# Kernel tuning notes

Hardware: AMD Instinct MI355X
Metric: run time of the kernel (lower is better)

Reference implementation:

```python
import jax, jax.numpy as jnp
import numpy as np

H = 2048      # hidden size
E = 16        # num experts
F = 1408      # per-expert ffn
FS = 4096     # shared expert ffn
B, S = 2, 1024


def setup_inputs() -> dict:
    key = jax.random.key(0)
    ks = jax.random.split(key, 9)
    s = 0.02
    x = jax.random.normal(ks[0], (B, S, H), dtype=jnp.float32)
    w_router = jax.random.normal(ks[1], (E, H), dtype=jnp.float32) * s
    Wg = jax.random.normal(ks[2], (E, H, F), dtype=jnp.float32) * s
    Wu = jax.random.normal(ks[3], (E, H, F), dtype=jnp.float32) * s
    Wd = jax.random.normal(ks[4], (E, F, H), dtype=jnp.float32) * s
    Wg_s = jax.random.normal(ks[5], (H, FS), dtype=jnp.float32) * s
    Wu_s = jax.random.normal(ks[6], (H, FS), dtype=jnp.float32) * s
    Wd_s = jax.random.normal(ks[7], (FS, H), dtype=jnp.float32) * s
    return {"x": x, "w_router": w_router, "Wg": Wg, "Wu": Wu, "Wd": Wd,
            "Wg_s": Wg_s, "Wu_s": Wu_s, "Wd_s": Wd_s, "top_k": 4}


def reference(x, w_router, Wg, Wu, Wd, Wg_s, Wu_s, Wd_s, top_k):
    # router: softmax in fp32, top-k, renormalize
    logits = jnp.einsum('bsh,eh->bse', x, w_router)
    probs = jax.nn.softmax(logits.astype(jnp.float32), axis=-1)
    w, idx = jax.lax.top_k(probs, top_k)            # [B,S,K]
    w = w / jnp.sum(w, axis=-1, keepdims=True)
    # per-token weight per expert; top-k experts are distinct, so the
    # per-slot masked loop in torch collapses to a single mask [B,S,E]
    mask = jnp.sum(jax.nn.one_hot(idx, E, dtype=w.dtype) * w[..., None], axis=-2)
    out = jnp.zeros_like(x)
    for e in range(E):
        m = mask[..., e:e + 1]                      # [B,S,1]
        xi = x * m                                  # input scaled by routing weight (matches torch)
        h = jax.nn.silu(jnp.einsum('bsh,hf->bsf', xi, Wg[e])) \
            * jnp.einsum('bsh,hf->bsf', xi, Wu[e])
        out = out + jnp.einsum('bsf,fh->bsh', h, Wd[e]) * m
    # shared expert (always active, unscaled)
    hs = jax.nn.silu(jnp.einsum('bsh,hf->bsf', x, Wg_s)) \
         * jnp.einsum('bsh,hf->bsf', x, Wu_s)
    out = out + jnp.einsum('bsf,fh->bsh', hs, Wd_s)
    return out
```

## Files before the change

kernel.cpp:

```cpp
#include <hip/hip_runtime.h>

#define H 2048
#define E 16
#define F 1408
#define FS 4096
#define T 2048
#define TOPK 4
#define CAP 2048
#define LDA 40
#define NPADROWS (T * TOPK + E * 128)

typedef __bf16 bf16;
typedef bf16 bf16x4 __attribute__((ext_vector_type(4)));
typedef bf16 bf16x8 __attribute__((ext_vector_type(8)));
typedef float floatx4 __attribute__((ext_vector_type(4)));

static __device__ __forceinline__ floatx4 mfma16(bf16x8 a, bf16x8 b, floatx4 c) {
    return __builtin_amdgcn_mfma_f32_16x16x32_bf16(a, b, c, 0, 0, 0);
}

static __device__ __forceinline__ void gload16(const bf16* g, bf16* l) {
    __builtin_amdgcn_global_load_lds(
        (const __attribute__((address_space(1))) void*)g,
        (__attribute__((address_space(3))) void*)l, 16, 0, 0);
}

__global__ __launch_bounds__(256) void router_kernel(
    const float* __restrict__ x, const float* __restrict__ wr,
    int* __restrict__ cnt, int* __restrict__ tokid, float* __restrict__ tokw) {
    const int wave = threadIdx.x >> 6;
    const int lane = threadIdx.x & 63;
    const int t = blockIdx.x * 4 + wave;
    if (t >= T) return;
    const float* xrow = x + (size_t)t * H;
    float xr[H / 64];
#pragma unroll
    for (int i = 0; i < H / 64; i++) xr[i] = xrow[lane + i * 64];
    float logits[E];
    for (int e = 0; e < E; e++) {
        const float* wrow = wr + (size_t)e * H;
        float p = 0.f;
#pragma unroll
        for (int i = 0; i < H / 64; i++) p += xr[i] * wrow[lane + i * 64];
        for (int off = 32; off; off >>= 1) p += __shfl_xor(p, off, 64);
        logits[e] = p;
    }
    float mx = logits[0];
    for (int e = 1; e < E; e++) mx = fmaxf(mx, logits[e]);
    float pr[E];
    float sum = 0.f;
    for (int e = 0; e < E; e++) { pr[e] = __expf(logits[e] - mx); sum += pr[e]; }
    float inv = 1.f / sum;
    for (int e = 0; e < E; e++) pr[e] *= inv;
    int sel[TOPK]; float sw[TOPK]; float wsum = 0.f;
    for (int k = 0; k < TOPK; k++) {
        float best = -1.f; int bi = 0;
        for (int e = 0; e < E; e++) if (pr[e] > best) { best = pr[e]; bi = e; }
        sel[k] = bi; sw[k] = best; wsum += best; pr[bi] = -2.f;
    }
    if (lane == 0) {
        float invw = 1.f / wsum;
        for (int k = 0; k < TOPK; k++) {
            int e = sel[k];
            int pos = atomicAdd(&cnt[e], 1);
            tokid[e * CAP + pos] = t;
            tokw[e * CAP + pos] = sw[k] * invw;
        }
    }
}

__global__ void prefix_kernel(const int* __restrict__ cnt, int* __restrict__ prefix, int pad) {
    if (threadIdx.x == 0) {
        int s = 0;
        for (int e = 0; e < E; e++) {
            prefix[e] = s;
            int c = cnt[e];
            s += pad ? ((c + 127) & ~127) : c;
        }
        prefix[E] = s;
    }
}

__global__ __launch_bounds__(256) void convert_x(const float* __restrict__ x,
                                                 bf16* __restrict__ Xb) {
    const int t = threadIdx.x;
    const int row = blockIdx.x * 8 + (t >> 5);
    const int l32 = t & 31;
    const float* src = x + (size_t)row * H;
    bf16* dst = Xb + (size_t)row * H;
    const int xk = (row & 3) << 3;
#pragma unroll
    for (int i = 0; i < 8; i++) {
        int kb = l32 * 8 + i * 256;
        float4 a = *(const float4*)(src + kb);
        float4 b = *(const float4*)(src + kb + 4);
        bf16x8 v;
        v[0] = (bf16)a.x; v[1] = (bf16)a.y; v[2] = (bf16)a.z; v[3] = (bf16)a.w;
        v[4] = (bf16)b.x; v[5] = (bf16)b.y; v[6] = (bf16)b.z; v[7] = (bf16)b.w;
        *(bf16x8*)(dst + (kb ^ xk)) = v;
    }
}

__global__ __launch_bounds__(256) void gather_x(
    const float* __restrict__ x, const int* __restrict__ cnt,
    const int* __restrict__ prefixPad, const int* __restrict__ tokid,
    const float* __restrict__ tokw, bf16* __restrict__ Xg) {
    const int e = blockIdx.y;
    const int s0 = blockIdx.x * 8;
    const int n = cnt[e];
    if (s0 >= n) return;
    const int t = threadIdx.x;
    const int sl = s0 + (t >> 5);
    const int l32 = t & 31;
    if (sl >= n) return;
    const int tok = tokid[e * CAP + sl];
    const float w = tokw[e * CAP + sl];
    const int row = prefixPad[e] + sl;
    const float* src = x + (size_t)tok * H;
    bf16* dst = Xg + (size_t)row * H;
    const int xk = (row & 3) << 3;
#pragma unroll
    for (int i = 0; i < 8; i++) {
        int kb = l32 * 8 + i * 256;
        float4 a = *(const float4*)(src + kb);
        float4 b = *(const float4*)(src + kb + 4);
        bf16x8 v;
        v[0] = (bf16)(a.x * w); v[1] = (bf16)(a.y * w);
        v[2] = (bf16)(a.z * w); v[3] = (bf16)(a.w * w);
        v[4] = (bf16)(b.x * w); v[5] = (bf16)(b.y * w);
        v[6] = (bf16)(b.z * w); v[7] = (bf16)(b.w * w);
        *(bf16x8*)(dst + (kb ^ xk)) = v;
    }
}

__global__ __launch_bounds__(256) void transpose_cvt(
    const float* __restrict__ src, bf16* __restrict__ dst, int R, int C) {
    __shared__ bf16 tile[32][36];
    const int t = threadIdx.x;
    const size_t zb = (size_t)blockIdx.z * R * C;
    const int r0 = blockIdx.y * 32, c0 = blockIdx.x * 32;
    {
        const int rl = t >> 3, c4 = (t & 7) * 4;
        float4 v = *(const float4*)(src + zb + (size_t)(r0 + rl) * C + c0 + c4);
        tile[rl][c4 + 0] = (bf16)v.x;
        tile[rl][c4 + 1] = (bf16)v.y;
        tile[rl][c4 + 2] = (bf16)v.z;
        tile[rl][c4 + 3] = (bf16)v.w;
    }
    __syncthreads();
    {
        const int cl = t >> 3, r4 = (t & 7) * 4;
        bf16x4 o;
        o[0] = tile[r4 + 0][cl];
        o[1] = tile[r4 + 1][cl];
        o[2] = tile[r4 + 2][cl];
        o[3] = tile[r4 + 3][cl];
        const int cg = c0 + cl;
        *(bf16x4*)(dst + zb + (size_t)cg * R + ((r0 + r4) ^ ((cg & 3) << 3))) = o;
    }
}

template <bool EXPERT>
__global__ __launch_bounds__(256, 2) void s1_gemm(
    const bf16* __restrict__ Abuf, const bf16* __restrict__ BgT,
    const bf16* __restrict__ BuT, bf16* __restrict__ hout,
    const int* __restrict__ cnt, const int* __restrict__ prefixPad, int nF) {
    __shared__ __align__(16) bf16 As[128 * 32];
    __shared__ __align__(16) bf16 Bgs[128 * 32];
    __shared__ __align__(16) bf16 Bus[128 * 32];
    const int tid = threadIdx.x;
    const int n0 = blockIdx.x * 128;
    const int m0 = blockIdx.y * 128;
    int ne = T;
    const bf16* A = Abuf;
    const bf16* bg = BgT;
    const bf16* bu = BuT;
    bf16* hb = hout;
    if (EXPERT) {
        const int e = blockIdx.z;
        ne = cnt[e];
        if (m0 >= ne) return;
        const int pp = prefixPad[e];
        A = Abuf + (size_t)pp * H;
        bg = BgT + (size_t)e * F * H;
        bu = BuT + (size_t)e * F * H;
        hb = hout + (size_t)pp * F;
    }
    const int lane = tid & 63;
    const int wave = tid >> 6;
    const int sr = wave * 32 + (lane >> 2);
    const int sc = (lane & 3) * 8;
    const int lo = wave * 1024;
    const bf16* aSrc = A + (size_t)(m0 + sr) * H + sc;
    const bf16* gSrc = bg + (size_t)(n0 + sr) * H + sc;
    const bf16* uSrc = bu + (size_t)(n0 + sr) * H + sc;

    const int m_ = lane & 15;
    const int quad = lane >> 4;
    const int wm = (wave & 1) * 64;
    const int wn = (wave >> 1) * 64;
    const int xq = (quad ^ (m_ & 3)) << 3;

    floatx4 accg[4][4], accu[4][4];
#pragma unroll
    for (int i = 0; i < 4; i++)
#pragma unroll
        for (int j = 0; j < 4; j++) {
            accg[i][j] = (floatx4){0.f, 0.f, 0.f, 0.f};
            accu[i][j] = (floatx4){0.f, 0.f, 0.f, 0.f};
        }

    for (int k0 = 0; k0 < H; k0 += 32) {
        gload16(aSrc + k0, &As[lo]);
        gload16(aSrc + k0 + (size_t)16 * H, &As[lo + 512]);
        gload16(gSrc + k0, &Bgs[lo]);
        gload16(gSrc + k0 + (size_t)16 * H, &Bgs[lo + 512]);
        gload16(uSrc + k0, &Bus[lo]);
        gload16(uSrc + k0 + (size_t)16 * H, &Bus[lo + 512]);
        __syncthreads();
        bf16x8 af[4], bgf[4], buf_[4];
#pragma unroll
        for (int mi = 0; mi < 4; mi++)
            af[mi] = *(const bf16x8*)&As[(wm + mi * 16 + m_) * 32 + xq];
#pragma unroll
        for (int ni = 0; ni < 4; ni++) {
            bgf[ni] = *(const bf16x8*)&Bgs[(wn + ni * 16 + m_) * 32 + xq];
            buf_[ni] = *(const bf16x8*)&Bus[(wn + ni * 16 + m_) * 32 + xq];
        }
#pragma unroll
        for (int mi = 0; mi < 4; mi++)
#pragma unroll
            for (int ni = 0; ni < 4; ni++) {
                accg[mi][ni] = mfma16(af[mi], bgf[ni], accg[mi][ni]);
                accu[mi][ni] = mfma16(af[mi], buf_[ni], accu[mi][ni]);
            }
        __syncthreads();
    }

#pragma unroll
    for (int mi = 0; mi < 4; mi++)
#pragma unroll
        for (int ni = 0; ni < 4; ni++)
#pragma unroll
            for (int r = 0; r < 4; r++) {
                int row = m0 + wm + mi * 16 + quad * 4 + r;
                int col = n0 + wn + ni * 16 + m_;
                if (!EXPERT || row < ne) {
                    float g = accg[mi][ni][r];
                    float u = accu[mi][ni][r];
                    float hv = g / (1.f + __expf(-g)) * u;
                    hb[(size_t)row * nF + (col ^ ((row & 3) << 3))] = (bf16)hv;
                }
            }
}

template <bool EXPERT>
__global__ __launch_bounds__(256, 3) void s2_gemm(
    const bf16* __restrict__ hin, const bf16* __restrict__ BdT,
    float* __restrict__ out, const int* __restrict__ cnt,
    const int* __restrict__ prefixPad, const int* __restrict__ tokid,
    const float* __restrict__ tokw, int nK) {
    __shared__ __align__(16) bf16 As[128 * 32];
    __shared__ __align__(16) bf16 Bs[128 * 32];
    const int tid = threadIdx.x;
    const int n0 = blockIdx.x * 128;
    const int m0 = blockIdx.y * 128;
    int ne = T;
    const bf16* hb = hin;
    const bf16* bd = BdT;
    int e = 0;
    if (EXPERT) {
        e = blockIdx.z;
        ne = cnt[e];
        if (m0 >= ne) return;
        hb = hin + (size_t)prefixPad[e] * F;
        bd = BdT + (size_t)e * F * H;
    }
    const int lane = tid & 63;
    const int wave = tid >> 6;
    const int sr = wave * 32 + (lane >> 2);
    const int sc = (lane & 3) * 8;
    const int lo = wave * 1024;
    const bf16* aSrc = hb + (size_t)(m0 + sr) * nK + sc;
    const bf16* bSrc = bd + (size_t)(n0 + sr) * nK + sc;

    const int m_ = lane & 15;
    const int quad = lane >> 4;
    const int wm = (wave & 1) * 64;
    const int wn = (wave >> 1) * 64;
    const int xq = (quad ^ (m_ & 3)) << 3;

    floatx4 acc[4][4];
#pragma unroll
    for (int i = 0; i < 4; i++)
#pragma unroll
        for (int j = 0; j < 4; j++) acc[i][j] = (floatx4){0.f, 0.f, 0.f, 0.f};

    for (int k0 = 0; k0 < nK; k0 += 32) {
        gload16(aSrc + k0, &As[lo]);
        gload16(aSrc + k0 + (size_t)16 * nK, &As[lo + 512]);
        gload16(bSrc + k0, &Bs[lo]);
        gload16(bSrc + k0 + (size_t)16 * nK, &Bs[lo + 512]);
        __syncthreads();
        bf16x8 af[4], bf_[4];
#pragma unroll
        for (int mi = 0; mi < 4; mi++)
            af[mi] = *(const bf16x8*)&As[(wm + mi * 16 + m_) * 32 + xq];
#pragma unroll
        for (int ni = 0; ni < 4; ni++)
            bf_[ni] = *(const bf16x8*)&Bs[(wn + ni * 16 + m_) * 32 + xq];
#pragma unroll
        for (int mi = 0; mi < 4; mi++)
#pragma unroll
            for (int ni = 0; ni < 4; ni++)
                acc[mi][ni] = mfma16(af[mi], bf_[ni], acc[mi][ni]);
        __syncthreads();
    }

#pragma unroll
    for (int mi = 0; mi < 4; mi++)
#pragma unroll
        for (int ni = 0; ni < 4; ni++)
#pragma unroll
            for (int r = 0; r < 4; r++) {
                int row = m0 + wm + mi * 16 + quad * 4 + r;
                int col = n0 + wn + ni * 16 + m_;
                if (EXPERT) {
                    if (row < ne) {
                        int t = tokid[e * CAP + row];
                        float wgt = tokw[e * CAP + row];
                        atomicAdd(out + (size_t)t * H + col, acc[mi][ni][r] * wgt);
                    }
                } else {
                    out[(size_t)row * H + col] = acc[mi][ni][r];
                }
            }
}

template <bool EXPERT>
__global__ __launch_bounds__(256) void stage1_gemm(
    const float* __restrict__ x, const float* __restrict__ wg_all,
    const float* __restrict__ wu_all, bf16* __restrict__ hout,
    const int* __restrict__ cnt, const int* __restrict__ prefix,
    const int* __restrict__ tokid, const float* __restrict__ tokw, int nF) {
    __shared__ __align__(16) bf16 As[128 * LDA];
    __shared__ __align__(16) bf16 Bg[128 * LDA];
    __shared__ __align__(16) bf16 Bu[128 * LDA];
    const int tid = threadIdx.x;
    const int n0 = blockIdx.x * 128;
    const int m0 = blockIdx.y * 128;
    int e = 0, ne = T;
    const float* wg = wg_all;
    const float* wu = wu_all;
    bf16* hb = hout;
    if (EXPERT) {
        e = blockIdx.z;
        ne = cnt[e];
        if (m0 >= ne) return;
        wg = wg_all + (size_t)e * H * F;
        wu = wu_all + (size_t)e * H * F;
        hb = hout + (size_t)prefix[e] * F;
    }
    const float* aptr[4]; float ascl[4]; bool avalid[4];
#pragma unroll
    for (int j = 0; j < 4; j++) {
        int idx = tid + j * 256;
        int r = idx >> 3;
        int kq = (idx & 7) * 4;
        int slot = m0 + r;
        if (EXPERT) {
            if (slot < ne) {
                int t = tokid[e * CAP + slot];
                aptr[j] = x + (size_t)t * H + kq;
                ascl[j] = tokw[e * CAP + slot];
                avalid[j] = true;
            } else { aptr[j] = x; ascl[j] = 0.f; avalid[j] = false; }
        } else {
            aptr[j] = x + (size_t)slot * H + kq;
            ascl[j] = 1.f; avalid[j] = true;
        }
    }
    const int lane = tid & 63;
    const int m = lane & 15;
    const int quad = lane >> 4;
    const int wave = tid >> 6;
    const int wm = (wave & 1) * 64;
    const int wn = (wave >> 1) * 64;
    floatx4 accg[4][4], accu[4][4];
#pragma unroll
    for (int i = 0; i < 4; i++)
#pragma unroll
        for (int j = 0; j < 4; j++) {
            accg[i][j] = (floatx4){0.f, 0.f, 0.f, 0.f};
            accu[i][j] = (floatx4){0.f, 0.f, 0.f, 0.f};
        }
    for (int k0 = 0; k0 < H; k0 += 32) {
#pragma unroll
        for (int j = 0; j < 4; j++) {
            int idx = tid + j * 256;
            int r = idx >> 3;
            int kq = (idx & 7) * 4;
            float4 v = make_float4(0.f, 0.f, 0.f, 0.f);
            if (!EXPERT || avalid[j]) v = *(const float4*)(aptr[j] + k0);
            bf16x4 bv;
            bv[0] = (bf16)(v.x * ascl[j]); bv[1] = (bf16)(v.y * ascl[j]);
            bv[2] = (bf16)(v.z * ascl[j]); bv[3] = (bf16)(v.w * ascl[j]);
            *(bf16x4*)&As[r * LDA + kq] = bv;
        }
#pragma unroll
        for (int j = 0; j < 4; j++) {
            int idx = tid + j * 256;
            int kk = idx >> 5;
            int n4 = (idx & 31) * 4;
            float4 vg = *(const float4*)(wg + (size_t)(k0 + kk) * nF + n0 + n4);
            Bg[(n4 + 0) * LDA + kk] = (bf16)vg.x;
            Bg[(n4 + 1) * LDA + kk] = (bf16)vg.y;
            Bg[(n4 + 2) * LDA + kk] = (bf16)vg.z;
            Bg[(n4 + 3) * LDA + kk] = (bf16)vg.w;
            float4 vu = *(const float4*)(wu + (size_t)(k0 + kk) * nF + n0 + n4);
            Bu[(n4 + 0) * LDA + kk] = (bf16)vu.x;
            Bu[(n4 + 1) * LDA + kk] = (bf16)vu.y;
            Bu[(n4 + 2) * LDA + kk] = (bf16)vu.z;
            Bu[(n4 + 3) * LDA + kk] = (bf16)vu.w;
        }
        __syncthreads();
        bf16x8 af[4], bgf[4], buf_[4];
#pragma unroll
        for (int mi = 0; mi < 4; mi++)
            af[mi] = *(const bf16x8*)&As[(wm + mi * 16 + m) * LDA + quad * 8];
#pragma unroll
        for (int ni = 0; ni < 4; ni++) {
            bgf[ni] = *(const bf16x8*)&Bg[(wn + ni * 16 + m) * LDA + quad * 8];
            buf_[ni] = *(const bf16x8*)&Bu[(wn + ni * 16 + m) * LDA + quad * 8];
        }
#pragma unroll
        for (int mi = 0; mi < 4; mi++)
#pragma unroll
            for (int ni = 0; ni < 4; ni++) {
                accg[mi][ni] = mfma16(af[mi], bgf[ni], accg[mi][ni]);
                accu[mi][ni] = mfma16(af[mi], buf_[ni], accu[mi][ni]);
            }
        __syncthreads();
    }
#pragma unroll
    for (int mi = 0; mi < 4; mi++)
#pragma unroll
        for (int ni = 0; ni < 4; ni++)
#pragma unroll
            for (int r = 0; r < 4; r++) {
                int row = m0 + wm + mi * 16 + quad * 4 + r;
                int col = n0 + wn + ni * 16 + m;
                if (!EXPERT || row < ne) {
                    float g = accg[mi][ni][r];
                    float u = accu[mi][ni][r];
                    float hv = g / (1.f + __expf(-g)) * u;
                    hb[(size_t)row * nF + col] = (bf16)hv;
                }
            }
}

template <bool EXPERT>
__global__ __launch_bounds__(256) void stage2_gemm(
    const bf16* __restrict__ hin, const float* __restrict__ wd_all,
    float* __restrict__ out, const int* __restrict__ cnt,
    const int* __restrict__ prefix, const int* __restrict__ tokid,
    const float* __restrict__ tokw, int nK) {
    __shared__ __align__(16) bf16 As[128 * LDA];
    __shared__ __align__(16) bf16 Bs[128 * LDA];
    const int tid = threadIdx.x;
    const int n0 = blockIdx.x * 128;
    const int m0 = blockIdx.y * 128;
    int e = 0, ne = T;
    const float* wd = wd_all;
    const bf16* hb = hin;
    if (EXPERT) {
        e = blockIdx.z;
        ne = cnt[e];
        if (m0 >= ne) return;
        wd = wd_all + (size_t)e * F * H;
        hb = hin + (size_t)prefix[e] * F;
    }
    const int lane = tid & 63;
    const int m = lane & 15;
    const int quad = lane >> 4;
    const int wave = tid >> 6;
    const int wm = (wave & 1) * 64;
    const int wn = (wave >> 1) * 64;
    floatx4 acc[4][4];
#pragma unroll
    for (int i = 0; i < 4; i++)
#pragma unroll
        for (int j = 0; j < 4; j++) acc[i][j] = (floatx4){0.f, 0.f, 0.f, 0.f};
    for (int k0 = 0; k0 < nK; k0 += 32) {
#pragma unroll
        for (int j = 0; j < 2; j++) {
            int idx = tid + j * 256;
            int r = idx >> 2;
            int k8 = (idx & 3) * 8;
            bf16x8 v;
#pragma unroll
            for (int q = 0; q < 8; q++) v[q] = (bf16)0.f;
            int row = m0 + r;
            if (!EXPERT || row < ne)
                v = *(const bf16x8*)(hb + (size_t)row * nK + k0 + k8);
            *(bf16x8*)&As[r * LDA + k8] = v;
        }
#pragma unroll
        for (int j = 0; j < 4; j++) {
            int idx = tid + j * 256;
            int kk = idx >> 5;
            int n4 = (idx & 31) * 4;
            float4 v = *(const float4*)(wd + (size_t)(k0 + kk) * H + n0 + n4);
            Bs[(n4 + 0) * LDA + kk] = (bf16)v.x;
            Bs[(n4 + 1) * LDA + kk] = (bf16)v.y;
            Bs[(n4 + 2) * LDA + kk] = (bf16)v.z;
            Bs[(n4 + 3) * LDA + kk] = (bf16)v.w;
        }
        __syncthreads();
        bf16x8 af[4], bf_[4];
#pragma unroll
        for (int mi = 0; mi < 4; mi++)
            af[mi] = *(const bf16x8*)&As[(wm + mi * 16 + m) * LDA + quad * 8];
#pragma unroll
        for (int ni = 0; ni < 4; ni++)
            bf_[ni] = *(const bf16x8*)&Bs[(wn + ni * 16 + m) * LDA + quad * 8];
#pragma unroll
        for (int mi = 0; mi < 4; mi++)
#pragma unroll
            for (int ni = 0; ni < 4; ni++)
                acc[mi][ni] = mfma16(af[mi], bf_[ni], acc[mi][ni]);
        __syncthreads();
    }
#pragma unroll
    for (int mi = 0; mi < 4; mi++)
#pragma unroll
        for (int ni = 0; ni < 4; ni++)
#pragma unroll
            for (int r = 0; r < 4; r++) {
                int row = m0 + wm + mi * 16 + quad * 4 + r;
                int col = n0 + wn + ni * 16 + m;
                if (EXPERT) {
                    if (row < ne) {
                        int t = tokid[e * CAP + row];
                        float wgt = tokw[e * CAP + row];
                        atomicAdd(out + (size_t)t * H + col, acc[mi][ni][r] * wgt);
                    }
                } else {
                    out[(size_t)row * H + col] = acc[mi][ni][r];
                }
            }
}

extern "C" void kernel_launch(void* const* d_in, const int* in_sizes, int n_in,
                              void* d_out, int out_size, void* d_ws, size_t ws_size,
                              hipStream_t stream) {
    const float* x = (const float*)d_in[0];
    const float* w_router = (const float*)d_in[1];
    const float* Wg = (const float*)d_in[2];
    const float* Wu = (const float*)d_in[3];
    const float* Wd = (const float*)d_in[4];
    const float* Wg_s = (const float*)d_in[5];
    const float* Wu_s = (const float*)d_in[6];
    const float* Wd_s = (const float*)d_in[7];
    float* out = (float*)d_out;

    char* w = (char*)d_ws;
    int* cnt = (int*)(w + 0);
    int* prefix = (int*)(w + 64);
    int* tokid = (int*)(w + 256);
    float* tokw = (float*)(w + 256 + (size_t)E * CAP * 4);

    constexpr size_t OFF_XB = 262400;
    constexpr size_t OFF_XG = OFF_XB + (size_t)T * H * 2;
    constexpr size_t OFF_HS = OFF_XG + (size_t)NPADROWS * H * 2;
    constexpr size_t OFF_HB = OFF_HS + (size_t)T * FS * 2;
    constexpr size_t OFF_WGT = OFF_HB + (size_t)NPADROWS * F * 2;
    constexpr size_t OFF_WUT = OFF_WGT + (size_t)E * F * H * 2;
    constexpr size_t OFF_WDT = OFF_WUT + (size_t)E * F * H * 2;
    constexpr size_t OFF_WGS = OFF_WDT + (size_t)E * F * H * 2;
    constexpr size_t OFF_WUS = OFF_WGS + (size_t)H * FS * 2;
    constexpr size_t OFF_WDS = OFF_WUS + (size_t)H * FS * 2;
    constexpr size_t WS_NEED = OFF_WDS + (size_t)H * FS * 2;

    hipMemsetAsync(cnt, 0, 64, stream);
    router_kernel<<<T / 4, 256, 0, stream>>>(x, w_router, cnt, tokid, tokw);

    if (ws_size >= WS_NEED) {
        bf16* Xb = (bf16*)(w + OFF_XB);
        bf16* Xg = (bf16*)(w + OFF_XG);
        bf16* Hs = (bf16*)(w + OFF_HS);
        bf16* Hb = (bf16*)(w + OFF_HB);
        bf16* WgT = (bf16*)(w + OFF_WGT);
        bf16* WuT = (bf16*)(w + OFF_WUT);
        bf16* WdT = (bf16*)(w + OFF_WDT);
        bf16* WgsT = (bf16*)(w + OFF_WGS);
        bf16* WusT = (bf16*)(w + OFF_WUS);
        bf16* WdsT = (bf16*)(w + OFF_WDS);

        prefix_kernel<<<1, 64, 0, stream>>>(cnt, prefix, 1);
        convert_x<<<T / 8, 256, 0, stream>>>(x, Xb);
        gather_x<<<dim3(CAP / 8, E), 256, 0, stream>>>(x, cnt, prefix, tokid, tokw, Xg);
        transpose_cvt<<<dim3(F / 32, H / 32, E), 256, 0, stream>>>(Wg, WgT, H, F);
        transpose_cvt<<<dim3(F / 32, H / 32, E), 256, 0, stream>>>(Wu, WuT, H, F);
        transpose_cvt<<<dim3(H / 32, F / 32, E), 256, 0, stream>>>(Wd, WdT, F, H);
        transpose_cvt<<<dim3(FS / 32, H / 32, 1), 256, 0, stream>>>(Wg_s, WgsT, H, FS);
        transpose_cvt<<<dim3(FS / 32, H / 32, 1), 256, 0, stream>>>(Wu_s, WusT, H, FS);
        transpose_cvt<<<dim3(H / 32, FS / 32, 1), 256, 0, stream>>>(Wd_s, WdsT, FS, H);

        s1_gemm<false><<<dim3(FS / 128, T / 128, 1), 256, 0, stream>>>(
            Xb, WgsT, WusT, Hs, nullptr, nullptr, FS);
        s1_gemm<true><<<dim3(F / 128, CAP / 128, E), 256, 0, stream>>>(
            Xg, WgT, WuT, Hb, cnt, prefix, F);
        s2_gemm<false><<<dim3(H / 128, T / 128, 1), 256, 0, stream>>>(
            Hs, WdsT, out, nullptr, nullptr, nullptr, nullptr, FS);
        s2_gemm<true><<<dim3(H / 128, CAP / 128, E), 256, 0, stream>>>(
            Hb, WdT, out, cnt, prefix, tokid, tokw, F);
    } else {
        bf16* Hs = (bf16*)(w + 262400);
        bf16* Hb = (bf16*)(w + 262400 + (size_t)T * FS * 2);

        prefix_kernel<<<1, 64, 0, stream>>>(cnt, prefix, 0);
        stage1_gemm<false><<<dim3(FS / 128, T / 128, 1), 256, 0, stream>>>(
            x, Wg_s, Wu_s, Hs, nullptr, nullptr, nullptr, nullptr, FS);
        stage1_gemm<true><<<dim3(F / 128, T / 128, E), 256, 0, stream>>>(
            x, Wg, Wu, Hb, cnt, prefix, tokid, tokw, F);
        stage2_gemm<false><<<dim3(H / 128, T / 128, 1), 256, 0, stream>>>(
            Hs, Wd_s, out, nullptr, nullptr, nullptr, nullptr, FS);
        stage2_gemm<true><<<dim3(H / 128, T / 128, E), 256, 0, stream>>>(
            Hb, Wd, out, cnt, prefix, tokid, tokw, F);
    }
}
```

Baseline: 1.260 ms.

## Merge stage-1 GEMMs into one flat-grid launch with K=64 tiles and compacted expert blocks

Merges the shared and expert gate/up GEMMs into one launch. It uses a flattened grid that maps blocks onto only the padded rows actually occupied, with an interleaved block-id remap for cache locality, so the many early-exit blocks of the per-expert 3D grid go away. The K tile grows from 32 to 64 with an 8-way XOR swizzle, which halves barriers per K and widens the loads. The weight transpose now handles 64-row tiles with 8-wide stores. The change doubles LDS per block, which may limit occupancy in s2 (launch bounds go from 3 to 2), and it drops the fp32 fallback path.

Result: faster. 1.175 ms (-6.8%).

```diff
diff --git a/kernel.cpp b/kernel.cpp
--- a/kernel.cpp
+++ b/kernel.cpp
@@ -7,8 +7,11 @@
 #define T 2048
 #define TOPK 4
 #define CAP 2048
-#define LDA 40
 #define NPADROWS (T * TOPK + E * 128)
+#define NMB (NPADROWS / 128)
+#define NS ((FS / 128) * (T / 128))
+#define GS1 (NS + (F / 128) * NMB)
+#define GS2E ((H / 128) * NMB)
 
 typedef __bf16 bf16;
 typedef bf16 bf16x4 __attribute__((ext_vector_type(4)));
@@ -69,14 +72,10 @@
     }
 }
 
-__global__ void prefix_kernel(const int* __restrict__ cnt, int* __restrict__ prefix, int pad) {
+__global__ void prefix_kernel(const int* __restrict__ cnt, int* __restrict__ prefix) {
     if (threadIdx.x == 0) {
         int s = 0;
-        for (int e = 0; e < E; e++) {
-            prefix[e] = s;
-            int c = cnt[e];
-            s += pad ? ((c + 127) & ~127) : c;
-        }
+        for (int e = 0; e < E; e++) { prefix[e] = s; s += (cnt[e] + 127) & ~127; }
         prefix[E] = s;
     }
 }
@@ -88,7 +87,7 @@
     const int l32 = t & 31;
     const float* src = x + (size_t)row * H;
     bf16* dst = Xb + (size_t)row * H;
-    const int xk = (row & 3) << 3;
+    const int xk = (row & 7) << 3;
 #pragma unroll
     for (int i = 0; i < 8; i++) {
         int kb = l32 * 8 + i * 256;
@@ -118,7 +117,7 @@
     const int row = prefixPad[e] + sl;
     const float* src = x + (size_t)tok * H;
     bf16* dst = Xg + (size_t)row * H;
-    const int xk = (row & 3) << 3;
+    const int xk = (row & 7) << 3;
 #pragma unroll
     for (int i = 0; i < 8; i++) {
         int kb = l32 * 8 + i * 256;
@@ -135,71 +134,83 @@
 
 __global__ __launch_bounds__(256) void transpose_cvt(
     const float* __restrict__ src, bf16* __restrict__ dst, int R, int C) {
-    __shared__ bf16 tile[32][36];
+    __shared__ float tile[64][33];
     const int t = threadIdx.x;
     const size_t zb = (size_t)blockIdx.z * R * C;
-    const int r0 = blockIdx.y * 32, c0 = blockIdx.x * 32;
+    const int r0 = blockIdx.y * 64, c0 = blockIdx.x * 32;
     {
-        const int rl = t >> 3, c4 = (t & 7) * 4;
-        float4 v = *(const float4*)(src + zb + (size_t)(r0 + rl) * C + c0 + c4);
-        tile[rl][c4 + 0] = (bf16)v.x;
-        tile[rl][c4 + 1] = (bf16)v.y;
-        tile[rl][c4 + 2] = (bf16)v.z;
-        tile[rl][c4 + 3] = (bf16)v.w;
+        const int rl = t >> 2, c8 = (t & 3) * 8;
+        const float* s = src + zb + (size_t)(r0 + rl) * C + c0 + c8;
+        float4 v0 = *(const float4*)s;
+        float4 v1 = *(const float4*)(s + 4);
+        tile[rl][c8 + 0] = v0.x; tile[rl][c8 + 1] = v0.y;
+        tile[rl][c8 + 2] = v0.z; tile[rl][c8 + 3] = v0.w;
+        tile[rl][c8 + 4] = v1.x; tile[rl][c8 + 5] = v1.y;
+        tile[rl][c8 + 6] = v1.z; tile[rl][c8 + 7] = v1.w;
     }
     __syncthreads();
     {
-        const int cl = t >> 3, r4 = (t & 7) * 4;
-        bf16x4 o;
-        o[0] = tile[r4 + 0][cl];
-        o[1] = tile[r4 + 1][cl];
-        o[2] = tile[r4 + 2][cl];
-        o[3] = tile[r4 + 3][cl];
+        const int cl = t >> 3, r8 = (t & 7) * 8;
+        bf16x8 o;
+#pragma unroll
+        for (int i = 0; i < 8; i++) o[i] = (bf16)tile[r8 + i][cl];
         const int cg = c0 + cl;
-        *(bf16x4*)(dst + zb + (size_t)cg * R + ((r0 + r4) ^ ((cg & 3) << 3))) = o;
-    }
-}
-
-template <bool EXPERT>
-__global__ __launch_bounds__(256, 2) void s1_gemm(
-    const bf16* __restrict__ Abuf, const bf16* __restrict__ BgT,
-    const bf16* __restrict__ BuT, bf16* __restrict__ hout,
-    const int* __restrict__ cnt, const int* __restrict__ prefixPad, int nF) {
-    __shared__ __align__(16) bf16 As[128 * 32];
-    __shared__ __align__(16) bf16 Bgs[128 * 32];
-    __shared__ __align__(16) bf16 Bus[128 * 32];
+        *(bf16x8*)(dst + zb + (size_t)cg * R + ((r0 + r8) ^ ((cg & 7) << 3))) = o;
+    }
+}
+
+__global__ __launch_bounds__(256, 2) void s1_all(
+    const bf16* __restrict__ Xb, const bf16* __restrict__ Xg,
+    const bf16* __restrict__ WgsT, const bf16* __restrict__ WusT,
+    const bf16* __restrict__ WgT, const bf16* __restrict__ WuT,
+    bf16* __restrict__ Hs, bf16* __restrict__ Hb,
+    const int* __restrict__ cnt, const int* __restrict__ prefixPad) {
+    __shared__ __align__(16) bf16 As[128 * 64];
+    __shared__ __align__(16) bf16 Bgs[128 * 64];
+    __shared__ __align__(16) bf16 Bus[128 * 64];
+
+    const int raw = blockIdx.x;
+    const int id = (raw & 7) * (GS1 / 8) + (raw >> 3);
+
+    int n0, m0, ne, nF;
+    const bf16 *A, *bg, *bu;
+    bf16* hb;
+    if (id < NS) {
+        m0 = (id & 15) * 128;
+        n0 = (id >> 4) * 128;
+        ne = 1 << 30;
+        nF = FS;
+        A = Xb; bg = WgsT; bu = WusT; hb = Hs;
+    } else {
+        const int id2 = id - NS;
+        const int mb = id2 % NMB;
+        const int xx = id2 / NMB;
+        const int rowbase = mb * 128;
+        if (rowbase >= prefixPad[E]) return;
+        int e = 0;
+        while (prefixPad[e + 1] <= rowbase) e++;
+        const int pp = prefixPad[e];
+        m0 = rowbase - pp;
+        ne = cnt[e];
+        n0 = xx * 128;
+        nF = F;
+        A = Xg + (size_t)pp * H;
+        bg = WgT + (size_t)e * F * H;
+        bu = WuT + (size_t)e * F * H;
+        hb = Hb + (size_t)pp * F;
+    }
+
     const int tid = threadIdx.x;
-    const int n0 = blockIdx.x * 128;
-    const int m0 = blockIdx.y * 128;
-    int ne = T;
-    const bf16* A = Abuf;
-    const bf16* bg = BgT;
-    const bf16* bu = BuT;
-    bf16* hb = hout;
-    if (EXPERT) {
-        const int e = blockIdx.z;
-        ne = cnt[e];
-        if (m0 >= ne) return;
-        const int pp = prefixPad[e];
-        A = Abuf + (size_t)pp * H;
-        bg = BgT + (size_t)e * F * H;
-        bu = BuT + (size_t)e * F * H;
-        hb = hout + (size_t)pp * F;
-    }
     const int lane = tid & 63;
     const int wave = tid >> 6;
-    const int sr = wave * 32 + (lane >> 2);
-    const int sc = (lane & 3) * 8;
-    const int lo = wave * 1024;
-    const bf16* aSrc = A + (size_t)(m0 + sr) * H + sc;
-    const bf16* gSrc = bg + (size_t)(n0 + sr) * H + sc;
-    const bf16* uSrc = bu + (size_t)(n0 + sr) * H + sc;
+    const bf16* aP = A + (size_t)(m0 + wave * 32 + (lane >> 3)) * H + (lane & 7) * 8;
+    const bf16* gP = bg + (size_t)(n0 + wave * 32 + (lane >> 3)) * H + (lane & 7) * 8;
+    const bf16* uP = bu + (size_t)(n0 + wave * 32 + (lane >> 3)) * H + (lane & 7) * 8;
 
     const int m_ = lane & 15;
     const int quad = lane >> 4;
     const int wm = (wave & 1) * 64;
     const int wn = (wave >> 1) * 64;
-    const int xq = (quad ^ (m_ & 3)) << 3;
 
     floatx4 accg[4][4], accu[4][4];
 #pragma unroll
@@ -210,30 +221,34 @@
             accu[i][j] = (floatx4){0.f, 0.f, 0.f, 0.f};
         }
 
-    for (int k0 = 0; k0 < H; k0 += 32) {
-        gload16(aSrc + k0, &As[lo]);
-        gload16(aSrc + k0 + (size_t)16 * H, &As[lo + 512]);
-        gload16(gSrc + k0, &Bgs[lo]);
-        gload16(gSrc + k0 + (size_t)16 * H, &Bgs[lo + 512]);
-        gload16(uSrc + k0, &Bus[lo]);
-        gload16(uSrc + k0 + (size_t)16 * H, &Bus[lo + 512]);
+    for (int k0 = 0; k0 < H; k0 += 64) {
+#pragma unroll
+        for (int j = 0; j < 4; j++) {
+            gload16(aP + k0 + (size_t)j * 8 * H, &As[wave * 2048 + j * 512]);
+            gload16(gP + k0 + (size_t)j * 8 * H, &Bgs[wave * 2048 + j * 512]);
+            gload16(uP + k0 + (size_t)j * 8 * H, &Bus[wave * 2048 + j * 512]);
+        }
         __syncthreads();
-        bf16x8 af[4], bgf[4], buf_[4];
-#pragma unroll
-        for (int mi = 0; mi < 4; mi++)
-            af[mi] = *(const bf16x8*)&As[(wm + mi * 16 + m_) * 32 + xq];
-#pragma unroll
-        for (int ni = 0; ni < 4; ni++) {
-            bgf[ni] = *(const bf16x8*)&Bgs[(wn + ni * 16 + m_) * 32 + xq];
-            buf_[ni] = *(const bf16x8*)&Bus[(wn + ni * 16 + m_) * 32 + xq];
-        }
-#pragma unroll
-        for (int mi = 0; mi < 4; mi++)
+#pragma unroll
+        for (int kk = 0; kk < 2; kk++) {
+            const int ko = (((kk << 2) | quad) ^ (m_ & 7)) << 3;
+            bf16x8 af[4], bgf[4], buf_[4];
+#pragma unroll
+            for (int mi = 0; mi < 4; mi++)
+                af[mi] = *(const bf16x8*)&As[(wm + mi * 16 + m_) * 64 + ko];
 #pragma unroll
             for (int ni = 0; ni < 4; ni++) {
-                accg[mi][ni] = mfma16(af[mi], bgf[ni], accg[mi][ni]);
-                accu[mi][ni] = mfma16(af[mi], buf_[ni], accu[mi][ni]);
+                bgf[ni] = *(const bf16x8*)&Bgs[(wn + ni * 16 + m_) * 64 + ko];
+                buf_[ni] = *(const bf16x8*)&Bus[(wn + ni * 16 + m_) * 64 + ko];
             }
+#pragma unroll
+            for (int mi = 0; mi < 4; mi++)
+#pragma unroll
+                for (int ni = 0; ni < 4; ni++) {
+                    accg[mi][ni] = mfma16(af[mi], bgf[ni], accg[mi][ni]);
+                    accu[mi][ni] = mfma16(af[mi], buf_[ni], accu[mi][ni]);
+                }
+        }
         __syncthreads();
     }
 
@@ -245,50 +260,56 @@
             for (int r = 0; r < 4; r++) {
                 int row = m0 + wm + mi * 16 + quad * 4 + r;
                 int col = n0 + wn + ni * 16 + m_;
-                if (!EXPERT || row < ne) {
+                if (row < ne) {
                     float g = accg[mi][ni][r];
                     float u = accu[mi][ni][r];
                     float hv = g / (1.f + __expf(-g)) * u;
-                    hb[(size_t)row * nF + (col ^ ((row & 3) << 3))] = (bf16)hv;
+                    hb[(size_t)row * nF + (col ^ ((row & 7) << 3))] = (bf16)hv;
                 }
             }
 }
 
 template <bool EXPERT>
-__global__ __launch_bounds__(256, 3) void s2_gemm(
+__global__ __launch_bounds__(256, 2) void s2_gemm(
     const bf16* __restrict__ hin, const bf16* __restrict__ BdT,
     float* __restrict__ out, const int* __restrict__ cnt,
     const int* __restrict__ prefixPad, const int* __restrict__ tokid,
     const float* __restrict__ tokw, int nK) {
-    __shared__ __align__(16) bf16 As[128 * 32];
-    __shared__ __align__(16) bf16 Bs[128 * 32];
+    __shared__ __align__(16) bf16 As[128 * 64];
+    __shared__ __align__(16) bf16 Bs[128 * 64];
+    const int raw = blockIdx.x;
+    const int id = EXPERT ? (raw & 7) * (GS2E / 8) + (raw >> 3)
+                          : (raw & 7) * 32 + (raw >> 3);
+    int n0, m0, ne, e = 0;
+    const bf16 *A, *B;
+    if (EXPERT) {
+        const int mb = id % NMB;
+        const int xx = id / NMB;
+        const int rowbase = mb * 128;
+        if (rowbase >= prefixPad[E]) return;
+        while (prefixPad[e + 1] <= rowbase) e++;
+        const int pp = prefixPad[e];
+        m0 = rowbase - pp;
+        ne = cnt[e];
+        n0 = xx * 128;
+        A = hin + (size_t)pp * F;
+        B = BdT + (size_t)e * F * H;
+    } else {
+        m0 = (id & 15) * 128;
+        n0 = (id >> 4) * 128;
+        ne = 1 << 30;
+        A = hin; B = BdT;
+    }
     const int tid = threadIdx.x;
-    const int n0 = blockIdx.x * 128;
-    const int m0 = blockIdx.y * 128;
-    int ne = T;
-    const bf16* hb = hin;
-    const bf16* bd = BdT;
-    int e = 0;
-    if (EXPERT) {
-        e = blockIdx.z;
-        ne = cnt[e];
-        if (m0 >= ne) return;
-        hb = hin + (size_t)prefixPad[e] * F;
-        bd = BdT + (size_t)e * F * H;
-    }
     const int lane = tid & 63;
     const int wave = tid >> 6;
-    const int sr = wave * 32 + (lane >> 2);
-    const int sc = (lane & 3) * 8;
-    const int lo = wave * 1024;
-    const bf16* aSrc = hb + (size_t)(m0 + sr) * nK + sc;
-    const bf16* bSrc = bd + (size_t)(n0 + sr) * nK + sc;
+    const bf16* aP = A + (size_t)(m0 + wave * 32 + (lane >> 3)) * nK + (lane & 7) * 8;
+    const bf16* bP = B + (size_t)(n0 + wave * 32 + (lane >> 3)) * nK + (lane & 7) * 8;
 
     const int m_ = lane & 15;
     const int quad = lane >> 4;
     const int wm = (wave & 1) * 64;
     const int wn = (wave >> 1) * 64;
-    const int xq = (quad ^ (m_ & 3)) << 3;
 
     floatx4 acc[4][4];
 #pragma unroll
@@ -296,24 +317,29 @@
 #pragma unroll
         for (int j = 0; j < 4; j++) acc[i][j] = (floatx4){0.f, 0.f, 0.f, 0.f};
 
-    for (int k0 = 0; k0 < nK; k0 += 32) {
-        gload16(aSrc + k0, &As[lo]);
-        gload16(aSrc + k0 + (size_t)16 * nK, &As[lo + 512]);
-        gload16(bSrc + k0, &Bs[lo]);
-        gload16(bSrc + k0 + (size_t)16 * nK, &Bs[lo + 512]);
+    for (int k0 = 0; k0 < nK; k0 += 64) {
+#pragma unroll
+        for (int j = 0; j < 4; j++) {
+            gload16(aP + k0 + (size_t)j * 8 * nK, &As[wave * 2048 + j * 512]);
+            gload16(bP + k0 + (size_t)j * 8 * nK, &Bs[wave * 2048 + j * 512]);
+        }
         __syncthreads();
-        bf16x8 af[4], bf_[4];
-#pragma unroll
-        for (int mi = 0; mi < 4; mi++)
-            af[mi] = *(const bf16x8*)&As[(wm + mi * 16 + m_) * 32 + xq];
-#pragma unroll
-        for (int ni = 0; ni < 4; ni++)
-            bf_[ni] = *(const bf16x8*)&Bs[(wn + ni * 16 + m_) * 32 + xq];
-#pragma unroll
-        for (int mi = 0; mi < 4; mi++)
+#pragma unroll
+        for (int kk = 0; kk < 2; kk++) {
+            const int ko = (((kk << 2) | quad) ^ (m_ & 7)) << 3;
+            bf16x8 af[4], bf_[4];
+#pragma unroll
+            for (int mi = 0; mi < 4; mi++)
+                af[mi] = *(const bf16x8*)&As[(wm + mi * 16 + m_) * 64 + ko];
 #pragma unroll
             for (int ni = 0; ni < 4; ni++)
-                acc[mi][ni] = mfma16(af[mi], bf_[ni], acc[mi][ni]);
+                bf_[ni] = *(const bf16x8*)&Bs[(wn + ni * 16 + m_) * 64 + ko];
+#pragma unroll
+            for (int mi = 0; mi < 4; mi++)
+#pragma unroll
+                for (int ni = 0; ni < 4; ni++)
+                    acc[mi][ni] = mfma16(af[mi], bf_[ni], acc[mi][ni]);
+        }
         __syncthreads();
     }
 
@@ -337,220 +363,6 @@
             }
 }
 
-template <bool EXPERT>
-__global__ __launch_bounds__(256) void stage1_gemm(
-    const float* __restrict__ x, const float* __restrict__ wg_all,
-    const float* __restrict__ wu_all, bf16* __restrict__ hout,
-    const int* __restrict__ cnt, const int* __restrict__ prefix,
-    const int* __restrict__ tokid, const float* __restrict__ tokw, int nF) {
-    __shared__ __align__(16) bf16 As[128 * LDA];
-    __shared__ __align__(16) bf16 Bg[128 * LDA];
-    __shared__ __align__(16) bf16 Bu[128 * LDA];
-    const int tid = threadIdx.x;
-    const int n0 = blockIdx.x * 128;
-    const int m0 = blockIdx.y * 128;
-    int e = 0, ne = T;
-    const float* wg = wg_all;
-    const float* wu = wu_all;
-    bf16* hb = hout;
-    if (EXPERT) {
-        e = blockIdx.z;
-        ne = cnt[e];
-        if (m0 >= ne) return;
-        wg = wg_all + (size_t)e * H * F;
-        wu = wu_all + (size_t)e * H * F;
-        hb = hout + (size_t)prefix[e] * F;
-    }
-    const float* aptr[4]; float ascl[4]; bool avalid[4];
-#pragma unroll
-    for (int j = 0; j < 4; j++) {
-        int idx = tid + j * 256;
-        int r = idx >> 3;
-        int kq = (idx & 7) * 4;
-        int slot = m0 + r;
-        if (EXPERT) {
-            if (slot < ne) {
-                int t = tokid[e * CAP + slot];
-                aptr[j] = x + (size_t)t * H + kq;
-                ascl[j] = tokw[e * CAP + slot];
-                avalid[j] = true;
-            } else { aptr[j] = x; ascl[j] = 0.f; avalid[j] = false; }
-        } else {
-            aptr[j] = x + (size_t)slot * H + kq;
-            ascl[j] = 1.f; avalid[j] = true;
-        }
-    }
-    const int lane = tid & 63;
-    const int m = lane & 15;
-    const int quad = lane >> 4;
-    const int wave = tid >> 6;
-    const int wm = (wave & 1) * 64;
-    const int wn = (wave >> 1) * 64;
-    floatx4 accg[4][4], accu[4][4];
-#pragma unroll
-    for (int i = 0; i < 4; i++)
-#pragma unroll
-        for (int j = 0; j < 4; j++) {
-            accg[i][j] = (floatx4){0.f, 0.f, 0.f, 0.f};
-            accu[i][j] = (floatx4){0.f, 0.f, 0.f, 0.f};
-        }
-    for (int k0 = 0; k0 < H; k0 += 32) {
-#pragma unroll
-        for (int j = 0; j < 4; j++) {
-            int idx = tid + j * 256;
-            int r = idx >> 3;
-            int kq = (idx & 7) * 4;
-            float4 v = make_float4(0.f, 0.f, 0.f, 0.f);
-            if (!EXPERT || avalid[j]) v = *(const float4*)(aptr[j] + k0);
-            bf16x4 bv;
-            bv[0] = (bf16)(v.x * ascl[j]); bv[1] = (bf16)(v.y * ascl[j]);
-            bv[2] = (bf16)(v.z * ascl[j]); bv[3] = (bf16)(v.w * ascl[j]);
-            *(bf16x4*)&As[r * LDA + kq] = bv;
-        }
-#pragma unroll
-        for (int j = 0; j < 4; j++) {
-            int idx = tid + j * 256;
-            int kk = idx >> 5;
-            int n4 = (idx & 31) * 4;
-            float4 vg = *(const float4*)(wg + (size_t)(k0 + kk) * nF + n0 + n4);
-            Bg[(n4 + 0) * LDA + kk] = (bf16)vg.x;
-            Bg[(n4 + 1) * LDA + kk] = (bf16)vg.y;
-            Bg[(n4 + 2) * LDA + kk] = (bf16)vg.z;
-            Bg[(n4 + 3) * LDA + kk] = (bf16)vg.w;
-            float4 vu = *(const float4*)(wu + (size_t)(k0 + kk) * nF + n0 + n4);
-            Bu[(n4 + 0) * LDA + kk] = (bf16)vu.x;
-            Bu[(n4 + 1) * LDA + kk] = (bf16)vu.y;
-            Bu[(n4 + 2) * LDA + kk] = (bf16)vu.z;
-            Bu[(n4 + 3) * LDA + kk] = (bf16)vu.w;
-        }
-        __syncthreads();
-        bf16x8 af[4], bgf[4], buf_[4];
-#pragma unroll
-        for (int mi = 0; mi < 4; mi++)
-            af[mi] = *(const bf16x8*)&As[(wm + mi * 16 + m) * LDA + quad * 8];
-#pragma unroll
-        for (int ni = 0; ni < 4; ni++) {
-            bgf[ni] = *(const bf16x8*)&Bg[(wn + ni * 16 + m) * LDA + quad * 8];
-            buf_[ni] = *(const bf16x8*)&Bu[(wn + ni * 16 + m) * LDA + quad * 8];
-        }
-#pragma unroll
-        for (int mi = 0; mi < 4; mi++)
-#pragma unroll
-            for (int ni = 0; ni < 4; ni++) {
-                accg[mi][ni] = mfma16(af[mi], bgf[ni], accg[mi][ni]);
-                accu[mi][ni] = mfma16(af[mi], buf_[ni], accu[mi][ni]);
-            }
-        __syncthreads();
-    }
-#pragma unroll
-    for (int mi = 0; mi < 4; mi++)
-#pragma unroll
-        for (int ni = 0; ni < 4; ni++)
-#pragma unroll
-            for (int r = 0; r < 4; r++) {
-                int row = m0 + wm + mi * 16 + quad * 4 + r;
-                int col = n0 + wn + ni * 16 + m;
-                if (!EXPERT || row < ne) {
-                    float g = accg[mi][ni][r];
-                    float u = accu[mi][ni][r];
-                    float hv = g / (1.f + __expf(-g)) * u;
-                    hb[(size_t)row * nF + col] = (bf16)hv;
-                }
-            }
-}
-
-template <bool EXPERT>
-__global__ __launch_bounds__(256) void stage2_gemm(
-    const bf16* __restrict__ hin, const float* __restrict__ wd_all,
-    float* __restrict__ out, const int* __restrict__ cnt,
-    const int* __restrict__ prefix, const int* __restrict__ tokid,
-    const float* __restrict__ tokw, int nK) {
-    __shared__ __align__(16) bf16 As[128 * LDA];
-    __shared__ __align__(16) bf16 Bs[128 * LDA];
-    const int tid = threadIdx.x;
-    const int n0 = blockIdx.x * 128;
-    const int m0 = blockIdx.y * 128;
-    int e = 0, ne = T;
-    const float* wd = wd_all;
-    const bf16* hb = hin;
-    if (EXPERT) {
-        e = blockIdx.z;
-        ne = cnt[e];
-        if (m0 >= ne) return;
-        wd = wd_all + (size_t)e * F * H;
-        hb = hin + (size_t)prefix[e] * F;
-    }
-    const int lane = tid & 63;
-    const int m = lane & 15;
-    const int quad = lane >> 4;
-    const int wave = tid >> 6;
-    const int wm = (wave & 1) * 64;
-    const int wn = (wave >> 1) * 64;
-    floatx4 acc[4][4];
-#pragma unroll
-    for (int i = 0; i < 4; i++)
-#pragma unroll
-        for (int j = 0; j < 4; j++) acc[i][j] = (floatx4){0.f, 0.f, 0.f, 0.f};
-    for (int k0 = 0; k0 < nK; k0 += 32) {
-#pragma unroll
-        for (int j = 0; j < 2; j++) {
-            int idx = tid + j * 256;
-            int r = idx >> 2;
-            int k8 = (idx & 3) * 8;
-            bf16x8 v;
-#pragma unroll
-            for (int q = 0; q < 8; q++) v[q] = (bf16)0.f;
-            int row = m0 + r;
-            if (!EXPERT || row < ne)
-                v = *(const bf16x8*)(hb + (size_t)row * nK + k0 + k8);
-            *(bf16x8*)&As[r * LDA + k8] = v;
-        }
-#pragma unroll
-        for (int j = 0; j < 4; j++) {
-            int idx = tid + j * 256;
-            int kk = idx >> 5;
-            int n4 = (idx & 31) * 4;
-            float4 v = *(const float4*)(wd + (size_t)(k0 + kk) * H + n0 + n4);
-            Bs[(n4 + 0) * LDA + kk] = (bf16)v.x;
-            Bs[(n4 + 1) * LDA + kk] = (bf16)v.y;
-            Bs[(n4 + 2) * LDA + kk] = (bf16)v.z;
-            Bs[(n4 + 3) * LDA + kk] = (bf16)v.w;
-        }
-        __syncthreads();
-        bf16x8 af[4], bf_[4];
-#pragma unroll
-        for (int mi = 0; mi < 4; mi++)
-            af[mi] = *(const bf16x8*)&As[(wm + mi * 16 + m) * LDA + quad * 8];
-#pragma unroll
-        for (int ni = 0; ni < 4; ni++)
-            bf_[ni] = *(const bf16x8*)&Bs[(wn + ni * 16 + m) * LDA + quad * 8];
-#pragma unroll
-        for (int mi = 0; mi < 4; mi++)
-#pragma unroll
-            for (int ni = 0; ni < 4; ni++)
-                acc[mi][ni] = mfma16(af[mi], bf_[ni], acc[mi][ni]);
-        __syncthreads();
-    }
-#pragma unroll
-    for (int mi = 0; mi < 4; mi++)
-#pragma unroll
-        for (int ni = 0; ni < 4; ni++)
-#pragma unroll
-            for (int r = 0; r < 4; r++) {
-                int row = m0 + wm + mi * 16 + quad * 4 + r;
-                int col = n0 + wn + ni * 16 + m;
-                if (EXPERT) {
-                    if (row < ne) {
-                        int t = tokid[e * CAP + row];
-                        float wgt = tokw[e * CAP + row];
-                        atomicAdd(out + (size_t)t * H + col, acc[mi][ni][r] * wgt);
-                    }
-                } else {
-                    out[(size_t)row * H + col] = acc[mi][ni][r];
-                }
-            }
-}
-
 extern "C" void kernel_launch(void* const* d_in, const int* in_sizes, int n_in,
                               void* d_out, int out_size, void* d_ws, size_t ws_size,
                               hipStream_t stream) {
@@ -580,53 +392,35 @@
     constexpr size_t OFF_WGS = OFF_WDT + (size_t)E * F * H * 2;
     constexpr size_t OFF_WUS = OFF_WGS + (size_t)H * FS * 2;
     constexpr size_t OFF_WDS = OFF_WUS + (size_t)H * FS * 2;
-    constexpr size_t WS_NEED = OFF_WDS + (size_t)H * FS * 2;
+
+    bf16* Xb = (bf16*)(w + OFF_XB);
+    bf16* Xg = (bf16*)(w + OFF_XG);
+    bf16* Hs = (bf16*)(w + OFF_HS);
+    bf16* Hb = (bf16*)(w + OFF_HB);
+    bf16* WgT = (bf16*)(w + OFF_WGT);
+    bf16* WuT = (bf16*)(w + OFF_WUT);
+    bf16* WdT = (bf16*)(w + OFF_WDT);
+    bf16* WgsT = (bf16*)(w + OFF_WGS);
+    bf16* WusT = (bf16*)(w + OFF_WUS);
+    bf16* WdsT = (bf16*)(w + OFF_WDS);
 
     hipMemsetAsync(cnt, 0, 64, stream);
     router_kernel<<<T / 4, 256, 0, stream>>>(x, w_router, cnt, tokid, tokw);
-
-    if (ws_size >= WS_NEED) {
-        bf16* Xb = (bf16*)(w + OFF_XB);
-        bf16* Xg = (bf16*)(w + OFF_XG);
-        bf16* Hs = (bf16*)(w + OFF_HS);
-        bf16* Hb = (bf16*)(w + OFF_HB);
-        bf16* WgT = (bf16*)(w + OFF_WGT);
-        bf16* WuT = (bf16*)(w + OFF_WUT);
-        bf16* WdT = (bf16*)(w + OFF_WDT);
-        bf16* WgsT = (bf16*)(w + OFF_WGS);
-        bf16* WusT = (bf16*)(w + OFF_WUS);
-        bf16* WdsT = (bf16*)(w + OFF_WDS);
-
-        prefix_kernel<<<1, 64, 0, stream>>>(cnt, prefix, 1);
-        convert_x<<<T / 8, 256, 0, stream>>>(x, Xb);
-        gather_x<<<dim3(CAP / 8, E), 256, 0, stream>>>(x, cnt, prefix, tokid, tokw, Xg);
-        transpose_cvt<<<dim3(F / 32, H / 32, E), 256, 0, stream>>>(Wg, WgT, H, F);
-        transpose_cvt<<<dim3(F / 32, H / 32, E), 256, 0, stream>>>(Wu, WuT, H, F);
-        transpose_cvt<<<dim3(H / 32, F / 32, E), 256, 0, stream>>>(Wd, WdT, F, H);
-        transpose_cvt<<<dim3(FS / 32, H / 32, 1), 256, 0, stream>>>(Wg_s, WgsT, H, FS);
-        transpose_cvt<<<dim3(FS / 32, H / 32, 1), 256, 0, stream>>>(Wu_s, WusT, H, FS);
-        transpose_cvt<<<dim3(H / 32, FS / 32, 1), 256, 0, stream>>>(Wd_s, WdsT, FS, H);
-
-        s1_gemm<false><<<dim3(FS / 128, T / 128, 1), 256, 0, stream>>>(
-            Xb, WgsT, WusT, Hs, nullptr, nullptr, FS);
-        s1_gemm<true><<<dim3(F / 128, CAP / 128, E), 256, 0, stream>>>(
-            Xg, WgT, WuT, Hb, cnt, prefix, F);
-        s2_gemm<false><<<dim3(H / 128, T / 128, 1), 256, 0, stream>>>(
-            Hs, WdsT, out, nullptr, nullptr, nullptr, nullptr, FS);
-        s2_gemm<true><<<dim3(H / 128, CAP / 128, E), 256, 0, stream>>>(
-            Hb, WdT, out, cnt, prefix, tokid, tokw, F);
-    } else {
-        bf16* Hs = (bf16*)(w + 262400);
-        bf16* Hb = (bf16*)(w + 262400 + (size_t)T * FS * 2);
-
-        prefix_kernel<<<1, 64, 0, stream>>>(cnt, prefix, 0);
-        stage1_gemm<false><<<dim3(FS / 128, T / 128, 1), 256, 0, stream>>>(
-            x, Wg_s, Wu_s, Hs, nullptr, nullptr, nullptr, nullptr, FS);
-        stage1_gemm<true><<<dim3(F / 128, T / 128, E), 256, 0, stream>>>(
-            x, Wg, Wu, Hb, cnt, prefix, tokid, tokw, F);
-        stage2_gemm<false><<<dim3(H / 128, T / 128, 1), 256, 0, stream>>>(
-            Hs, Wd_s, out, nullptr, nullptr, nullptr, nullptr, FS);
-        stage2_gemm<true><<<dim3(H / 128, T / 128, E), 256, 0, stream>>>(
-            Hb, Wd, out, cnt, prefix, tokid, tokw, F);
-    }
-}
+    prefix_kernel<<<1, 64, 0, stream>>>(cnt, prefix);
+
+    convert_x<<<T / 8, 256, 0, stream>>>(x, Xb);
+    gather_x<<<dim3(CAP / 8, E), 256, 0, stream>>>(x, cnt, prefix, tokid, tokw, Xg);
+    transpose_cvt<<<dim3(F / 32, H / 64, E), 256, 0, stream>>>(Wg, WgT, H, F);
+    transpose_cvt<<<dim3(F / 32, H / 64, E), 256, 0, stream>>>(Wu, WuT, H, F);
+    transpose_cvt<<<dim3(H / 32, F / 64, E), 256, 0, stream>>>(Wd, WdT, F, H);
+    transpose_cvt<<<dim3(FS / 32, H / 64, 1), 256, 0, stream>>>(Wg_s, WgsT, H, FS);
+    transpose_cvt<<<dim3(FS / 32, H / 64, 1), 256, 0, stream>>>(Wu_s, WusT, H, FS);
+    transpose_cvt<<<dim3(H / 32, FS / 64, 1), 256, 0, stream>>>(Wd_s, WdsT, FS, H);
+
+    s1_all<<<GS1, 256, 0, stream>>>(Xb, Xg, WgsT, WusT, WgT, WuT, Hs, Hb, cnt, prefix);
+
+    s2_gemm<false><<<(H / 128) * (T / 128), 256, 0, stream>>>(
+        Hs, WdsT, out, nullptr, nullptr, nullptr, nullptr, FS);
+    s2_gemm<true><<<GS2E, 256, 0, stream>>>(
+        Hb, WdT, out, cnt, prefix, tokid, tokw, F);
+}
```
